# Kernel tuning notes

Measured on AMD Instinct MI355X. Metric: run time of the kernel, lower is better.

Reference implementation:

```python
import jax, jax.numpy as jnp
import numpy as np

N = 50000
E = 800000
DZ = 64
DH = 64


def setup_inputs() -> dict:
    key = jax.random.key(0)
    ks = jax.random.split(key, 10)
    z = jax.random.normal(ks[0], (N, DZ), dtype=jnp.float32)
    edge_src = jax.random.randint(ks[1], (E,), 0, N, dtype=jnp.int32)
    edge_dst = jax.random.randint(ks[2], (E,), 0, N, dtype=jnp.int32)
    # weights: normal(0, 0.1); biases: uniform(-0.1, 0.1) as in the torch init
    W_cur = 0.1 * jax.random.normal(ks[3], (DH, DZ), dtype=jnp.float32)
    b_cur = jax.random.uniform(ks[4], (DH,), minval=-0.1, maxval=0.1, dtype=jnp.float32)
    W_nbr = 0.1 * jax.random.normal(ks[5], (DH, 2 * DZ), dtype=jnp.float32)
    b_nbr = jax.random.uniform(ks[6], (DH,), minval=-0.1, maxval=0.1, dtype=jnp.float32)
    W_out = 0.1 * jax.random.normal(ks[7], (DZ, 2 * DH), dtype=jnp.float32)
    b_out = jax.random.uniform(ks[8], (DZ,), minval=-0.1, maxval=0.1, dtype=jnp.float32)
    return {"z": z, "edge_src": edge_src, "edge_dst": edge_dst,
            "W_cur": W_cur, "b_cur": b_cur, "W_nbr": W_nbr, "b_nbr": b_nbr,
            "W_out": W_out, "b_out": b_out}


def reference(z, edge_src, edge_dst, W_cur, b_cur, W_nbr, b_nbr, W_out, b_out):
    # self branch: Sigmoid(Linear(dim_z -> dim_h))  [N, DH]
    curvv = jax.nn.sigmoid(z @ W_cur.T + b_cur)
    # per-edge: concat(z[center], z[neighbor]) -> Sigmoid(Linear)  [E, DH]
    e = jnp.concatenate([z[edge_dst], z[edge_src]], axis=-1)  # [E, 2*DZ]
    m = jax.nn.sigmoid(e @ W_nbr.T + b_nbr)
    # sum-aggregate messages per center node (isolated nodes -> zeros)
    nbrvv = jax.ops.segment_sum(m, edge_dst, num_segments=N)  # [N, DH]
    # fuse: Tanh(Linear(concat(cur, nbr) -> dim_z))
    h = jnp.concatenate([curvv, nbrvv], axis=-1)  # [N, 2*DH]
    dzdt = jnp.tanh(h @ W_out.T + b_out)
    return dzdt
```

## Files before the change

### kernel.cpp

```cpp
#include <hip/hip_runtime.h>
#include <math.h>

#define NN 50000
#define NE 800000
#define BSH 7
#define NBUCK 391
#define CAP 4096
#define CHUNK 4096
#define NCH ((NE + CHUNK - 1) / CHUNK)
#define K1B 782
#define EPT2 8
#define SENT 50000
#define NL2E -1.4426950408889634f

typedef float4 f4;
typedef float2 f2;
typedef unsigned short u16;
typedef unsigned int u32;

__device__ __forceinline__ float sigf(float x) {
    return __builtin_amdgcn_rcpf(1.0f + __expf(-x));
}

__device__ __forceinline__ float sigf2(float y) {
    float e;
    asm("v_exp_f32 %0, %1" : "=v"(e) : "v"(y));
    return __builtin_amdgcn_rcpf(1.0f + e);
}

__device__ __forceinline__ u16 f32_to_bf16_rne(float f) {
    unsigned u = __float_as_uint(f);
    u += 0x7FFFu + ((u >> 16) & 1u);
    return (u16)(u >> 16);
}

#define K1_WFLOATS (3 * 32 * 64 * 2)
__global__ __launch_bounds__(512, 4) void k1_sc(
    const float* __restrict__ z,
    const float* __restrict__ Wc, const float* __restrict__ bc,
    const float* __restrict__ Wn, const float* __restrict__ bn,
    float* __restrict__ P, u16* __restrict__ Qh, float* __restrict__ C,
    const int* __restrict__ esrc, const int* __restrict__ edst,
    int* __restrict__ gcur, u32* __restrict__ ebuf)
{
    const int tid = threadIdx.x;
    if (blockIdx.x < K1B) {
        __shared__ float sh[K1_WFLOATS + 8 * 256];
        f2* w2 = (f2*)sh;
        for (int j = tid; j < 3 * 32 * 64; j += 512) {
            const int m = j >> 11, r = j & 2047;
            const int k2 = r >> 6, h = r & 63;
            const float* s = (m == 0) ? (Wc + h * 64 + 2 * k2)
                                      : (Wn + h * 128 + (m - 1) * 64 + 2 * k2);
            w2[(m * 32 + k2) * 64 + h] = *(const f2*)s;
        }
        __syncthreads();

        const int lane = tid & 63;
        const int wid  = tid >> 6;
        f4* tile = (f4*)(sh + K1_WFLOATS) + wid * 64;
        const f2* wl0 = w2;
        const f2* wl1 = w2 + 32 * 64;
        const f2* wl2 = w2 + 2 * 32 * 64;
        const float bcur = bc[lane], bnbr = bn[lane];

        const int gw = blockIdx.x * 8 + wid;
        const int nw = K1B * 8;
        for (int chunk = gw; chunk < NN / 4; chunk += nw) {
            const int n0 = chunk * 4;
            tile[lane] = *(const f4*)(z + n0 * 64 + lane * 4);
            float a0[4], a1[4], a2[4];
            #pragma unroll
            for (int ni = 0; ni < 4; ++ni) { a0[ni] = 0.f; a1[ni] = 0.f; a2[ni] = 0.f; }
            #pragma unroll 2
            for (int k4 = 0; k4 < 16; ++k4) {
                const f2 w0a = wl0[(2 * k4) * 64 + lane], w0b = wl0[(2 * k4 + 1) * 64 + lane];
                const f2 w1a = wl1[(2 * k4) * 64 + lane], w1b = wl1[(2 * k4 + 1) * 64 + lane];
                const f2 w2a = wl2[(2 * k4) * 64 + lane], w2b = wl2[(2 * k4 + 1) * 64 + lane];
                #pragma unroll
                for (int ni = 0; ni < 4; ++ni) {
                    const f4 zz = tile[ni * 16 + k4];
                    a0[ni] = fmaf(w0b.y, zz.w, fmaf(w0b.x, zz.z, fmaf(w0a.y, zz.y, fmaf(w0a.x, zz.x, a0[ni]))));
                    a1[ni] = fmaf(w1b.y, zz.w, fmaf(w1b.x, zz.z, fmaf(w1a.y, zz.y, fmaf(w1a.x, zz.x, a1[ni]))));
                    a2[ni] = fmaf(w2b.y, zz.w, fmaf(w2b.x, zz.z, fmaf(w2a.y, zz.y, fmaf(w2a.x, zz.x, a2[ni]))));
                }
            }
            #pragma unroll
            for (int ni = 0; ni < 4; ++ni) {
                const int n = n0 + ni;
                C[n * 64 + lane]  = sigf(a0[ni] + bcur);
                P[n * 64 + lane]  = (a1[ni] + bnbr) * NL2E;
                Qh[n * 64 + lane] = f32_to_bf16_rne(a2[ni] * NL2E);
            }
        }
    } else {
        if (blockIdx.x == K1B && tid < 64) Qh[(size_t)SENT * 64 + tid] = 0x7F80u;

        __shared__ int cnt[NBUCK];
        __shared__ int gbase[NBUCK];
        __shared__ int lcur[NBUCK];
        for (int i = tid; i < NBUCK; i += 512) cnt[i] = 0;
        __syncthreads();

        const int base = (blockIdx.x - K1B) * CHUNK;
        u32 ent[EPT2];
        int nb[EPT2];
        #pragma unroll
        for (int t = 0; t < EPT2; ++t) {
            const int e = base + t * 512 + tid;
            if (e < NE) {
                const int d = edst[e], s = esrc[e];
                const int b = d >> BSH;
                ent[t] = ((u32)(d & 127) << 16) | (u32)s;
                nb[t] = b;
                atomicAdd(&cnt[b], 1);
            } else {
                nb[t] = -1;
            }
        }
        __syncthreads();
        for (int i = tid; i < NBUCK; i += 512) {
            gbase[i] = cnt[i] ? atomicAdd(&gcur[i], cnt[i]) : 0;
            lcur[i] = 0;
        }
        __syncthreads();
        #pragma unroll
        for (int t = 0; t < EPT2; ++t) {
            if (nb[t] >= 0) {
                const int li = atomicAdd(&lcur[nb[t]], 1);
                ebuf[nb[t] * CAP + gbase[nb[t]] + li] = ent[t];
            }
        }
    }
}

__global__ __launch_bounds__(256) void k_bsort(const int* __restrict__ gcur,
                                               const u32* __restrict__ ebuf,
                                               u32* __restrict__ bd,
                                               u16* __restrict__ ss)
{
    __shared__ int hist[128];
    __shared__ int lcur[128];
    __shared__ int ps[128];
    __shared__ int tot;
    const int b = blockIdx.x;
    const int ecnt = gcur[b];
    const int e0 = b * CAP;
    const int n0 = b << BSH;
    const int t = threadIdx.x;

    if (t < 128) hist[t] = 0;
    __syncthreads();
    for (int j = t; j < ecnt; j += 256)
        atomicAdd(&hist[(ebuf[e0 + j] >> 16) & 127], 1);
    __syncthreads();
    if (t < 128) ps[t] = (hist[t] + 7) & ~7;
    __syncthreads();
    for (int o = 1; o < 128; o <<= 1) {
        int v = 0;
        if (t < 128 && t >= o) v = ps[t - o];
        __syncthreads();
        if (t < 128 && t >= o) ps[t] += v;
        __syncthreads();
    }
    if (t < 128) {
        const int a = hist[t];
        const int r = (a + 7) & ~7;
        const int excl = ps[t] - r;
        lcur[t] = excl;
        const int n = n0 + t;
        if (n < NN) bd[n] = ((u32)(e0 + excl) << 8) | (u32)a;
        if (t == 127) tot = ps[127];
    }
    __syncthreads();
    const int zw = (tot + 48) >> 1;
    u32* ssw = (u32*)(ss + e0);
    for (int j = t; j < zw; j += 256) ssw[j] = 0xC350C350u;
    __syncthreads();
    for (int j = t; j < ecnt; j += 256) {
        const u32 ent = ebuf[e0 + j];
        const int p = atomicAdd(&lcur[(ent >> 16) & 127], 1);
        ss[e0 + p] = (u16)(ent & 0xFFFFu);
    }
}

template<int NW>
__device__ __forceinline__ void round_g2(const u16* __restrict__ ip,
                                         const u16* __restrict__ qbl2,
                                         int sel, f2 p2,
                                         float& acc0, float& acc1)
{
    uint4 iv0, iv1, iv2;
    asm volatile("global_load_dwordx4 %0, %1, off" : "=v"(iv0) : "v"(ip));
    if constexpr (NW >= 8)
        asm volatile("global_load_dwordx4 %0, %1, off offset:16" : "=v"(iv1) : "v"(ip));
    if constexpr (NW >= 12)
        asm volatile("global_load_dwordx4 %0, %1, off offset:32" : "=v"(iv2) : "v"(ip));
    asm volatile("s_waitcnt vmcnt(0)" ::: "memory");
    __builtin_amdgcn_sched_barrier(0);
    u32 wv[NW];
    wv[0] = iv0.x; wv[1] = iv0.y; wv[2] = iv0.z; wv[3] = iv0.w;
    if constexpr (NW >= 8)  { wv[4] = iv1.x; wv[5] = iv1.y; wv[6] = iv1.z; wv[7] = iv1.w; }
    if constexpr (NW >= 12) { wv[8] = iv2.x; wv[9] = iv2.y; wv[10] = iv2.z; wv[11] = iv2.w; }
    u32 q[NW];
    #pragma unroll
    for (int w = 0; w < NW; ++w) {
        const u32 sv = (wv[w] >> sel) & 0xFFFFu;
        const u16* a = qbl2 + (sv << 6);
        asm volatile("global_load_dword %0, %1, off" : "=v"(q[w]) : "v"(a));
    }
    asm volatile("s_waitcnt vmcnt(0)" ::: "memory");
    __builtin_amdgcn_sched_barrier(0);
    #pragma unroll
    for (int w = 0; w < NW; ++w) {
        const float lo = __uint_as_float(q[w] << 16);
        const float hi = __uint_as_float(q[w] & 0xFFFF0000u);
        acc0 += sigf2(p2.x + lo);
        acc1 += sigf2(p2.y + hi);
    }
}

__global__ __launch_bounds__(512, 8) void k23(
    const u32* __restrict__ bd, const u16* __restrict__ ss,
    const float* __restrict__ P, const u16* __restrict__ Qh,
    const float* __restrict__ C, const float* __restrict__ Wo,
    const float* __restrict__ bo, float* __restrict__ out)
{
    __shared__ u32 w1u[32 * 64];
    __shared__ f2  w2f[32 * 64];
    __shared__ float tiles[8 * 512];
    const int tid = threadIdx.x;
    for (int j = tid; j < 32 * 64; j += 512) {
        const int k2 = j >> 6, d = j & 63;
        const f2 wc = *(const f2*)(Wo + d * 128 + 2 * k2);
        w1u[k2 * 64 + d] = ((u32)f32_to_bf16_rne(wc.y) << 16) | (u32)f32_to_bf16_rne(wc.x);
        w2f[k2 * 64 + d] = *(const f2*)(Wo + d * 128 + 64 + 2 * k2);
    }
    __syncthreads();

    const int lane = tid & 63;
    const int wid  = tid >> 6;
    float* tile = tiles + wid * 512;
    const f4* t4 = (const f4*)tile;
    const int sel = (lane >= 32) ? 16 : 0;
    const u16* qbl2 = Qh + (lane & 31) * 2;
    const float bout = bo[lane];

    for (int chunk = blockIdx.x * 8 + wid; chunk < NN / 4; chunk += gridDim.x * 8) {
        const int n0 = chunk * 4;
        #pragma unroll
        for (int i = 0; i < 4; ++i) {
            const int n = n0 + i;
            const u32 w = bd[n];
            const int beg = __builtin_amdgcn_readfirstlane((int)(w >> 8));
            const int dg  = __builtin_amdgcn_readfirstlane((int)(w & 255u));
            const int rdg = (dg + 7) & ~7;
            const f2 p2 = *(const f2*)(P + n * 64 + 2 * (lane & 31));
            tile[i * 128 + lane] = C[n * 64 + lane];
            float acc0 = 0.f, acc1 = 0.f;

            int jb = 0;
            for (; jb + 24 <= rdg; jb += 24)
                round_g2<12>(ss + beg + jb, qbl2, sel, p2, acc0, acc1);
            const int rem = rdg - jb;
            if (rem == 16)     round_g2<8>(ss + beg + jb, qbl2, sel, p2, acc0, acc1);
            else if (rem == 8) round_g2<4>(ss + beg + jb, qbl2, sel, p2, acc0, acc1);

            const float s0 = __shfl_xor(acc0, 32, 64);
            const float s1 = __shfl_xor(acc1, 32, 64);
            if (lane < 32) {
                f2 v; v.x = acc0 + s0; v.y = acc1 + s1;
                *(f2*)(tile + i * 128 + 64 + 2 * lane) = v;
            }
        }

        float a2[4] = {0.f, 0.f, 0.f, 0.f};
        #pragma unroll 2
        for (int k4 = 0; k4 < 16; ++k4) {
            const u32 ua = w1u[(2 * k4) * 64 + lane];
            const u32 ub = w1u[(2 * k4 + 1) * 64 + lane];
            const float wa0 = __uint_as_float(ua << 16);
            const float wa1 = __uint_as_float(ua & 0xFFFF0000u);
            const float wb0 = __uint_as_float(ub << 16);
            const float wb1 = __uint_as_float(ub & 0xFFFF0000u);
            #pragma unroll
            for (int i = 0; i < 4; ++i) {
                const f4 hv = t4[i * 32 + k4];
                a2[i] = fmaf(wb1, hv.w, fmaf(wb0, hv.z, fmaf(wa1, hv.y, fmaf(wa0, hv.x, a2[i]))));
            }
        }
        #pragma unroll 2
        for (int k4 = 0; k4 < 16; ++k4) {
            const f2 wa = w2f[(2 * k4) * 64 + lane];
            const f2 wb = w2f[(2 * k4 + 1) * 64 + lane];
            #pragma unroll
            for (int i = 0; i < 4; ++i) {
                const f4 hv = t4[i * 32 + 16 + k4];
                a2[i] = fmaf(wb.y, hv.w, fmaf(wb.x, hv.z, fmaf(wa.y, hv.y, fmaf(wa.x, hv.x, a2[i]))));
            }
        }
        #pragma unroll
        for (int i = 0; i < 4; ++i)
            out[(n0 + i) * 64 + lane] = tanhf(a2[i] + bout);
    }
}

extern "C" void kernel_launch(void* const* d_in, const int* in_sizes, int n_in,
                              void* d_out, int out_size, void* d_ws, size_t ws_size,
                              hipStream_t stream) {
    const float* z  = (const float*)d_in[0];
    const int* esrc = (const int*)d_in[1];
    const int* edst = (const int*)d_in[2];
    const float* Wc = (const float*)d_in[3];
    const float* bc = (const float*)d_in[4];
    const float* Wn = (const float*)d_in[5];
    const float* bn = (const float*)d_in[6];
    const float* Wo = (const float*)d_in[7];
    const float* bo = (const float*)d_in[8];
    float* out = (float*)d_out;

    float* P   = (float*)d_ws;
    float* C   = P + (size_t)NN * 64;
    u16* Qh    = (u16*)(C + (size_t)NN * 64);
    u32* bd    = (u32*)(Qh + (size_t)(NN + 1) * 64);
    int* gcur  = (int*)(bd + NN + 64);
    u32* ebuf  = (u32*)(gcur + 512);
    u16* ss    = (u16*)(ebuf + (size_t)NBUCK * CAP);

    hipMemsetAsync(gcur, 0, 512 * sizeof(int), stream);
    k1_sc<<<K1B + NCH, 512, 0, stream>>>(z, Wc, bc, Wn, bn, P, Qh, C,
                                         esrc, edst, gcur, ebuf);
    k_bsort<<<NBUCK, 256, 0, stream>>>(gcur, ebuf, bd, ss);
    k23<<<1563, 512, 0, stream>>>(bd, ss, P, Qh, C, Wo, bo, out);
}
```

Baseline: 102.7 us.

## Prefetch next node's edge indices while gathering current node's messages

```diff
diff --git a/kernel.cpp b/kernel.cpp
--- a/kernel.cpp
+++ b/kernel.cpp
@@ -12,6 +12,7 @@
 #define EPT2 8
 #define SENT 50000
 #define NL2E -1.4426950408889634f
+#define INFPAIR 0x7F807F80u
 
 typedef float4 f4;
 typedef float2 f2;
@@ -33,6 +34,13 @@
     u += 0x7FFFu + ((u >> 16) & 1u);
     return (u16)(u >> 16);
 }
+
+__device__ __forceinline__ u32 pack_bf16(f2 v) {
+    return ((u32)f32_to_bf16_rne(v.y) << 16) | (u32)f32_to_bf16_rne(v.x);
+}
+
+__device__ __forceinline__ float blo(u32 u) { return __uint_as_float(u << 16); }
+__device__ __forceinline__ float bhi(u32 u) { return __uint_as_float(u & 0xFFFF0000u); }
 
 #define K1_WFLOATS (3 * 32 * 64 * 2)
 __global__ __launch_bounds__(512, 4) void k1_sc(
@@ -181,6 +189,23 @@
         const u32 ent = ebuf[e0 + j];
         const int p = atomicAdd(&lcur[(ent >> 16) & 127], 1);
         ss[e0 + p] = (u16)(ent & 0xFFFFu);
+    }
+}
+
+#define IDX3(X0, X1, X2, ip) \
+    asm volatile("global_load_dwordx4 %0, %1, off"           : "=v"(X0) : "v"(ip)); \
+    asm volatile("global_load_dwordx4 %0, %1, off offset:16" : "=v"(X1) : "v"(ip)); \
+    asm volatile("global_load_dwordx4 %0, %1, off offset:32" : "=v"(X2) : "v"(ip));
+
+__device__ __forceinline__ void gath12(u32 (&q)[12], uint4 X0, uint4 X1, uint4 X2,
+                                       const u16* __restrict__ qbl2, int sel)
+{
+    const u32 wv[12] = {X0.x, X0.y, X0.z, X0.w, X1.x, X1.y, X1.z, X1.w,
+                        X2.x, X2.y, X2.z, X2.w};
+    #pragma unroll
+    for (int w = 0; w < 12; ++w) {
+        const u16* a = qbl2 + (((wv[w] >> sel) & 0xFFFFu) << 6);
+        asm volatile("global_load_dword %0, %1, off" : "=v"(q[w]) : "v"(a));
     }
 }
 
@@ -205,18 +230,15 @@
     u32 q[NW];
     #pragma unroll
     for (int w = 0; w < NW; ++w) {
-        const u32 sv = (wv[w] >> sel) & 0xFFFFu;
-        const u16* a = qbl2 + (sv << 6);
+        const u16* a = qbl2 + (((wv[w] >> sel) & 0xFFFFu) << 6);
         asm volatile("global_load_dword %0, %1, off" : "=v"(q[w]) : "v"(a));
     }
     asm volatile("s_waitcnt vmcnt(0)" ::: "memory");
     __builtin_amdgcn_sched_barrier(0);
     #pragma unroll
     for (int w = 0; w < NW; ++w) {
-        const float lo = __uint_as_float(q[w] << 16);
-        const float hi = __uint_as_float(q[w] & 0xFFFF0000u);
-        acc0 += sigf2(p2.x + lo);
-        acc1 += sigf2(p2.y + hi);
+        acc0 += sigf2(p2.x + blo(q[w]));
+        acc1 += sigf2(p2.y + bhi(q[w]));
     }
 }
 
@@ -232,8 +254,7 @@
     const int tid = threadIdx.x;
     for (int j = tid; j < 32 * 64; j += 512) {
         const int k2 = j >> 6, d = j & 63;
-        const f2 wc = *(const f2*)(Wo + d * 128 + 2 * k2);
-        w1u[k2 * 64 + d] = ((u32)f32_to_bf16_rne(wc.y) << 16) | (u32)f32_to_bf16_rne(wc.x);
+        w1u[k2 * 64 + d] = pack_bf16(*(const f2*)(Wo + d * 128 + 2 * k2));
         w2f[k2 * 64 + d] = *(const f2*)(Wo + d * 128 + 64 + 2 * k2);
     }
     __syncthreads();
@@ -243,33 +264,61 @@
     float* tile = tiles + wid * 512;
     const f4* t4 = (const f4*)tile;
     const int sel = (lane >= 32) ? 16 : 0;
+    const int odd = lane >> 5;
     const u16* qbl2 = Qh + (lane & 31) * 2;
     const float bout = bo[lane];
 
     for (int chunk = blockIdx.x * 8 + wid; chunk < NN / 4; chunk += gridDim.x * 8) {
         const int n0 = chunk * 4;
+        int beg[4], dg[4];
+        #pragma unroll
+        for (int i = 0; i < 4; ++i) {
+            const u32 w = bd[n0 + i];
+            beg[i] = __builtin_amdgcn_readfirstlane((int)(w >> 8));
+            dg[i]  = __builtin_amdgcn_readfirstlane((int)(w & 255u));
+        }
+
+        uint4 X0, X1, X2;
+        IDX3(X0, X1, X2, ss + beg[0]);
+
         #pragma unroll
         for (int i = 0; i < 4; ++i) {
             const int n = n0 + i;
-            const u32 w = bd[n];
-            const int beg = __builtin_amdgcn_readfirstlane((int)(w >> 8));
-            const int dg  = __builtin_amdgcn_readfirstlane((int)(w & 255u));
-            const int rdg = (dg + 7) & ~7;
             const f2 p2 = *(const f2*)(P + n * 64 + 2 * (lane & 31));
             tile[i * 128 + lane] = C[n * 64 + lane];
-            float acc0 = 0.f, acc1 = 0.f;
-
-            int jb = 0;
-            for (; jb + 24 <= rdg; jb += 24)
-                round_g2<12>(ss + beg + jb, qbl2, sel, p2, acc0, acc1);
-            const int rem = rdg - jb;
-            if (rem == 16)     round_g2<8>(ss + beg + jb, qbl2, sel, p2, acc0, acc1);
-            else if (rem == 8) round_g2<4>(ss + beg + jb, qbl2, sel, p2, acc0, acc1);
-
-            const float s0 = __shfl_xor(acc0, 32, 64);
-            const float s1 = __shfl_xor(acc1, 32, 64);
+
+            asm volatile("s_waitcnt vmcnt(0)" ::: "memory");
+            __builtin_amdgcn_sched_barrier(0);
+            u32 q[12];
+            gath12(q, X0, X1, X2, qbl2, sel);
+            if (i < 3) {
+                IDX3(X0, X1, X2, ss + beg[i + 1]);
+                asm volatile("s_waitcnt vmcnt(3)" ::: "memory");
+            } else {
+                asm volatile("s_waitcnt vmcnt(0)" ::: "memory");
+            }
+            __builtin_amdgcn_sched_barrier(0);
+
+            float o0 = 0.f, o1 = 0.f;
+            #pragma unroll
+            for (int w = 0; w < 12; ++w) {
+                const u32 qw = ((2 * w + odd) < dg[i]) ? q[w] : INFPAIR;
+                o0 += sigf2(p2.x + blo(qw));
+                o1 += sigf2(p2.y + bhi(qw));
+            }
+            if (dg[i] > 24) {
+                const int rdg = (dg[i] + 7) & ~7;
+                int jb = 24;
+                for (; jb + 24 <= rdg; jb += 24)
+                    round_g2<12>(ss + beg[i] + jb, qbl2, sel, p2, o0, o1);
+                const int rem = rdg - jb;
+                if (rem == 16)     round_g2<8>(ss + beg[i] + jb, qbl2, sel, p2, o0, o1);
+                else if (rem == 8) round_g2<4>(ss + beg[i] + jb, qbl2, sel, p2, o0, o1);
+            }
+            const float s0 = __shfl_xor(o0, 32, 64);
+            const float s1 = __shfl_xor(o1, 32, 64);
             if (lane < 32) {
-                f2 v; v.x = acc0 + s0; v.y = acc1 + s1;
+                f2 v; v.x = o0 + s0; v.y = o1 + s1;
                 *(f2*)(tile + i * 128 + 64 + 2 * lane) = v;
             }
         }
@@ -279,10 +328,8 @@
         for (int k4 = 0; k4 < 16; ++k4) {
             const u32 ua = w1u[(2 * k4) * 64 + lane];
             const u32 ub = w1u[(2 * k4 + 1) * 64 + lane];
-            const float wa0 = __uint_as_float(ua << 16);
-            const float wa1 = __uint_as_float(ua & 0xFFFF0000u);
-            const float wb0 = __uint_as_float(ub << 16);
-            const float wb1 = __uint_as_float(ub & 0xFFFF0000u);
+            const float wa0 = blo(ua), wa1 = bhi(ua);
+            const float wb0 = blo(ub), wb1 = bhi(ub);
             #pragma unroll
             for (int i = 0; i < 4; ++i) {
                 const f4 hv = t4[i * 32 + k4];
```

New measurement: 108.8 us. 1.06x slower.

## Gather four bf16 features per lane and split edges across four lane groups

Applied to the files above, without the earlier changes.

```diff
diff --git a/kernel.cpp b/kernel.cpp
--- a/kernel.cpp
+++ b/kernel.cpp
@@ -33,6 +33,13 @@
     u += 0x7FFFu + ((u >> 16) & 1u);
     return (u16)(u >> 16);
 }
+
+__device__ __forceinline__ u32 pack_bf16(f2 v) {
+    return ((u32)f32_to_bf16_rne(v.y) << 16) | (u32)f32_to_bf16_rne(v.x);
+}
+
+__device__ __forceinline__ float blo(u32 u) { return __uint_as_float(u << 16); }
+__device__ __forceinline__ float bhi(u32 u) { return __uint_as_float(u & 0xFFFF0000u); }
 
 #define K1_WFLOATS (3 * 32 * 64 * 2)
 __global__ __launch_bounds__(512, 4) void k1_sc(
@@ -184,39 +191,39 @@
     }
 }
 
-template<int NW>
-__device__ __forceinline__ void round_g2(const u16* __restrict__ ip,
-                                         const u16* __restrict__ qbl2,
-                                         int sel, f2 p2,
-                                         float& acc0, float& acc1)
+template<int NL>
+__device__ __forceinline__ void round_g4(const u16* __restrict__ ip,
+                                         const u16* __restrict__ qbl4,
+                                         int wofs, int sel, f4 p4,
+                                         float (&acc)[4])
 {
     uint4 iv0, iv1, iv2;
     asm volatile("global_load_dwordx4 %0, %1, off" : "=v"(iv0) : "v"(ip));
-    if constexpr (NW >= 8)
+    if constexpr (NL >= 4)
         asm volatile("global_load_dwordx4 %0, %1, off offset:16" : "=v"(iv1) : "v"(ip));
-    if constexpr (NW >= 12)
+    if constexpr (NL >= 6)
         asm volatile("global_load_dwordx4 %0, %1, off offset:32" : "=v"(iv2) : "v"(ip));
     asm volatile("s_waitcnt vmcnt(0)" ::: "memory");
     __builtin_amdgcn_sched_barrier(0);
-    u32 wv[NW];
+    u32 wv[2 * NL];
     wv[0] = iv0.x; wv[1] = iv0.y; wv[2] = iv0.z; wv[3] = iv0.w;
-    if constexpr (NW >= 8)  { wv[4] = iv1.x; wv[5] = iv1.y; wv[6] = iv1.z; wv[7] = iv1.w; }
-    if constexpr (NW >= 12) { wv[8] = iv2.x; wv[9] = iv2.y; wv[10] = iv2.z; wv[11] = iv2.w; }
-    u32 q[NW];
+    if constexpr (NL >= 4) { wv[4] = iv1.x; wv[5] = iv1.y; wv[6] = iv1.z; wv[7] = iv1.w; }
+    if constexpr (NL >= 6) { wv[8] = iv2.x; wv[9] = iv2.y; wv[10] = iv2.z; wv[11] = iv2.w; }
+    uint2 q[NL];
     #pragma unroll
-    for (int w = 0; w < NW; ++w) {
-        const u32 sv = (wv[w] >> sel) & 0xFFFFu;
-        const u16* a = qbl2 + (sv << 6);
-        asm volatile("global_load_dword %0, %1, off" : "=v"(q[w]) : "v"(a));
+    for (int j = 0; j < NL; ++j) {
+        const u32 w = wv[2 * j + wofs];
+        const u16* a = qbl4 + (((w >> sel) & 0xFFFFu) << 6);
+        asm volatile("global_load_dwordx2 %0, %1, off" : "=v"(q[j]) : "v"(a));
     }
     asm volatile("s_waitcnt vmcnt(0)" ::: "memory");
     __builtin_amdgcn_sched_barrier(0);
     #pragma unroll
-    for (int w = 0; w < NW; ++w) {
-        const float lo = __uint_as_float(q[w] << 16);
-        const float hi = __uint_as_float(q[w] & 0xFFFF0000u);
-        acc0 += sigf2(p2.x + lo);
-        acc1 += sigf2(p2.y + hi);
+    for (int j = 0; j < NL; ++j) {
+        acc[0] += sigf2(p4.x + blo(q[j].x));
+        acc[1] += sigf2(p4.y + bhi(q[j].x));
+        acc[2] += sigf2(p4.z + blo(q[j].y));
+        acc[3] += sigf2(p4.w + bhi(q[j].y));
     }
 }
 
@@ -232,8 +239,7 @@
     const int tid = threadIdx.x;
     for (int j = tid; j < 32 * 64; j += 512) {
         const int k2 = j >> 6, d = j & 63;
-        const f2 wc = *(const f2*)(Wo + d * 128 + 2 * k2);
-        w1u[k2 * 64 + d] = ((u32)f32_to_bf16_rne(wc.y) << 16) | (u32)f32_to_bf16_rne(wc.x);
+        w1u[k2 * 64 + d] = pack_bf16(*(const f2*)(Wo + d * 128 + 2 * k2));
         w2f[k2 * 64 + d] = *(const f2*)(Wo + d * 128 + 64 + 2 * k2);
     }
     __syncthreads();
@@ -242,8 +248,9 @@
     const int wid  = tid >> 6;
     float* tile = tiles + wid * 512;
     const f4* t4 = (const f4*)tile;
-    const int sel = (lane >= 32) ? 16 : 0;
-    const u16* qbl2 = Qh + (lane & 31) * 2;
+    const int wofs = lane >> 5;
+    const int sel  = ((lane >> 4) & 1) * 16;
+    const u16* qbl4 = Qh + (lane & 15) * 4;
     const float bout = bo[lane];
 
     for (int chunk = blockIdx.x * 8 + wid; chunk < NN / 4; chunk += gridDim.x * 8) {
@@ -255,22 +262,25 @@
             const int beg = __builtin_amdgcn_readfirstlane((int)(w >> 8));
             const int dg  = __builtin_amdgcn_readfirstlane((int)(w & 255u));
             const int rdg = (dg + 7) & ~7;
-            const f2 p2 = *(const f2*)(P + n * 64 + 2 * (lane & 31));
+            const f4 p4 = *(const f4*)(P + n * 64 + (lane & 15) * 4);
             tile[i * 128 + lane] = C[n * 64 + lane];
-            float acc0 = 0.f, acc1 = 0.f;
+            float acc[4] = {0.f, 0.f, 0.f, 0.f};
 
             int jb = 0;
             for (; jb + 24 <= rdg; jb += 24)
-                round_g2<12>(ss + beg + jb, qbl2, sel, p2, acc0, acc1);
+                round_g4<6>(ss + beg + jb, qbl4, wofs, sel, p4, acc);
             const int rem = rdg - jb;
-            if (rem == 16)     round_g2<8>(ss + beg + jb, qbl2, sel, p2, acc0, acc1);
-            else if (rem == 8) round_g2<4>(ss + beg + jb, qbl2, sel, p2, acc0, acc1);
-
-            const float s0 = __shfl_xor(acc0, 32, 64);
-            const float s1 = __shfl_xor(acc1, 32, 64);
-            if (lane < 32) {
-                f2 v; v.x = acc0 + s0; v.y = acc1 + s1;
-                *(f2*)(tile + i * 128 + 64 + 2 * lane) = v;
+            if (rem == 16)     round_g4<4>(ss + beg + jb, qbl4, wofs, sel, p4, acc);
+            else if (rem == 8) round_g4<2>(ss + beg + jb, qbl4, wofs, sel, p4, acc);
+
+            #pragma unroll
+            for (int t = 0; t < 4; ++t) {
+                acc[t] += __shfl_xor(acc[t], 16, 64);
+                acc[t] += __shfl_xor(acc[t], 32, 64);
+            }
+            if (lane < 16) {
+                f4 v; v.x = acc[0]; v.y = acc[1]; v.z = acc[2]; v.w = acc[3];
+                *(f4*)(tile + i * 128 + 64 + lane * 4) = v;
             }
         }
 
@@ -279,10 +289,8 @@
         for (int k4 = 0; k4 < 16; ++k4) {
             const u32 ua = w1u[(2 * k4) * 64 + lane];
             const u32 ub = w1u[(2 * k4 + 1) * 64 + lane];
-            const float wa0 = __uint_as_float(ua << 16);
-            const float wa1 = __uint_as_float(ua & 0xFFFF0000u);
-            const float wb0 = __uint_as_float(ub << 16);
-            const float wb1 = __uint_as_float(ub & 0xFFFF0000u);
+            const float wa0 = blo(ua), wa1 = bhi(ua);
+            const float wb0 = blo(ub), wb1 = bhi(ub);
             #pragma unroll
             for (int i = 0; i < 4; ++i) {
                 const f4 hv = t4[i * 32 + k4];
```

Measured after the change: 111.4 us. 8.6% more time.
